# Kernel tuning notes

Measured on AMD Instinct MI355X. Metric: run time of the kernel, lower is better.

The kernel has to match this reference:

```python
import jax, jax.numpy as jnp
import numpy as np

HIDDEN = 1024
RANK = 4
N_TASKS = 5
LORA_SCALING = 1.0 / RANK  # lora_alpha / lora_rank = 1/4
LN_EPS = 1e-5


def setup_inputs() -> dict:
    key = jax.random.key(0)
    ks = jax.random.split(key, 9)
    B, S, D = 16, 2048, HIDDEN
    hidden_states = jax.random.normal(ks[0], (B, S, D), dtype=jnp.float32)
    input_tensor = jax.random.normal(ks[1], (B, S, D), dtype=jnp.float32)
    adapter_mask = jax.random.randint(ks[2], (B,), 0, N_TASKS, dtype=jnp.int32)
    W = jax.random.normal(ks[3], (D, D), dtype=jnp.float32) * 0.02
    b = jax.random.normal(ks[4], (D,), dtype=jnp.float32) * 0.02
    lora_A = jax.random.normal(ks[5], (N_TASKS, RANK, D), dtype=jnp.float32) * 0.02
    lora_B = jax.random.normal(ks[6], (N_TASKS, D, RANK), dtype=jnp.float32) * 0.02
    gamma = jnp.ones((D,), dtype=jnp.float32)
    beta = jnp.zeros((D,), dtype=jnp.float32)
    return {
        "hidden_states": hidden_states,
        "input_tensor": input_tensor,
        "W": W,
        "b": b,
        "lora_A": lora_A,
        "lora_B": lora_B,
        "gamma": gamma,
        "beta": beta,
        "adapter_mask": adapter_mask,
    }


def _layernorm(x, gamma, beta):
    mu = jnp.mean(x, axis=-1, keepdims=True)
    xc = x - mu
    var = jnp.mean(xc * xc, axis=-1, keepdims=True)
    return xc * jax.lax.rsqrt(var + LN_EPS) * gamma + beta


def reference(hidden_states, input_tensor, W, b, lora_A, lora_B, gamma, beta, adapter_mask):
    # Base dense projection (first self.dense call)
    h1 = jnp.einsum("bsd,ed->bse", hidden_states, W) + b  # [B,S,D]
    # Per-task LoRA-parametrized dense applied to the projected states
    # (the source loops over unique tasks with gather/scatter; vectorized here
    #  by gathering each batch row's adapter).
    base2 = jnp.einsum("bsd,ed->bse", h1, W) + b  # [B,S,D]
    A_b = lora_A[adapter_mask]  # [B, r, D]
    B_b = lora_B[adapter_mask]  # [B, D, r]
    low = jnp.einsum("bsd,brd->bsr", h1, A_b)  # [B,S,r]
    delta = jnp.einsum("bsr,bdr->bsd", low, B_b)  # [B,S,D]
    h2 = base2 + LORA_SCALING * delta
    # dropout is identity in eval / p=0; residual + LayerNorm
    return _layernorm(h2 + input_tensor, gamma, beta)
```

## Files before the change

kernel.cpp:

```cpp
#include <hip/hip_runtime.h>
#include <hip/hip_bf16.h>
#include <stdint.h>

#define D_HID 1024
#define M_TOT 32768
#define LN_EPS 1e-5f

typedef __bf16 bf16x8 __attribute__((ext_vector_type(8)));
typedef float f32x4 __attribute__((ext_vector_type(4)));
typedef unsigned short u16;
typedef u16 u16x8 __attribute__((ext_vector_type(8)));
typedef u16 u16x4v __attribute__((ext_vector_type(4)));

__device__ __forceinline__ float bf2f(u16 x) {
  union { unsigned int u; float f; } c; c.u = ((unsigned int)x) << 16; return c.f;
}
__device__ __forceinline__ u16 f2bf(float f) {
  union { __bf16 h; u16 u; } c; c.h = (__bf16)f; return c.u;
}
__device__ __forceinline__ u16x8 cvt8(const float* g) {
  float4 f0 = *(const float4*)g;
  float4 f1 = *(const float4*)(g + 4);
  u16x8 v;
  v[0] = f2bf(f0.x); v[1] = f2bf(f0.y); v[2] = f2bf(f0.z); v[3] = f2bf(f0.w);
  v[4] = f2bf(f1.x); v[5] = f2bf(f1.y); v[6] = f2bf(f1.z); v[7] = f2bf(f1.w);
  return v;
}
__device__ __forceinline__ void gld16(const u16* g, u16* lds_wave_base) {
  __builtin_amdgcn_global_load_lds(
      (__attribute__((address_space(1))) unsigned int*)g,
      (__attribute__((address_space(3))) unsigned int*)lds_wave_base, 16, 0, 0);
}

__global__ __launch_bounds__(256) void s1_prep(
    const float* __restrict__ hs, u16* __restrict__ hs_bf,
    const float* __restrict__ W, u16* __restrict__ hi, u16* __restrict__ lo,
    u16* __restrict__ hiT, u16* __restrict__ loT,
    const float* __restrict__ lA, u16* __restrict__ lAh, u16* __restrict__ lAl) {
  __shared__ float tile[32][33];
  const int bid = blockIdx.x, tid = threadIdx.x;
  if (bid < 2048) {
    int i = bid * 256 + tid;
#pragma unroll
    for (int it = 0; it < 8; ++it, i += 2048 * 256)
      *(u16x8*)(hs_bf + (size_t)i * 8) = cvt8(hs + (size_t)i * 8);
    return;
  }
  if (bid >= 3072) {
    const int b = bid - 3072;
    for (int i = tid; i < 16 * 1024; i += 256) {
      const int r = b * 16 + (i >> 10), c = i & 1023;
      const float v = (r < 20) ? lA[(size_t)r * 1024 + c] : 0.f;
      const u16 h = f2bf(v);
      lAh[(size_t)r * 1024 + c] = h;
      lAl[(size_t)r * 1024 + c] = f2bf(v - bf2f(h));
    }
    return;
  }
  const int rb = bid - 2048;
  const int bj = rb & 31, bi = rb >> 5;
  const int tx = tid & 31, ty = tid >> 5;
#pragma unroll
  for (int r0 = 0; r0 < 32; r0 += 8) {
    const int r = r0 + ty;
    const size_t o = (size_t)(bi * 32 + r) * D_HID + bj * 32 + tx;
    const float v = W[o];
    tile[r][tx] = v;
    const u16 h = f2bf(v);
    hi[o] = h; lo[o] = f2bf(v - bf2f(h));
  }
  __syncthreads();
#pragma unroll
  for (int r0 = 0; r0 < 32; r0 += 8) {
    const int r = r0 + ty;
    const float v = tile[tx][r];
    const size_t o = (size_t)(bj * 32 + r) * D_HID + bi * 32 + tx;
    const u16 h = f2bf(v);
    hiT[o] = h; loT[o] = f2bf(v - bf2f(h));
  }
}

__global__ __launch_bounds__(256) void s2_gemm(
    const u16* __restrict__ Ah, const u16* __restrict__ Al,
    const u16* __restrict__ Bh, const u16* __restrict__ Bl,
    const u16* __restrict__ lAh, const u16* __restrict__ lAl,
    float* __restrict__ C, float* __restrict__ A2) {
  __shared__ __align__(16) u16 smem[4][64 * 32];
  const int bid = blockIdx.x, tid = threadIdx.x;
  const int wave = tid >> 6, lane = tid & 63;
  const int by = bid >> 4, bx = bid & 15;
  const bool isA2 = (by == 16);
  const u16* Asel_h = isA2 ? lAh : Ah;
  const u16* Asel_l = isA2 ? lAl : Al;
  const int arow0 = isA2 ? 0 : by * 64;
  const u16* gsel = (wave == 0) ? Asel_h : (wave == 1) ? Asel_l
                  : (wave == 2) ? Bh : Bl;
  const int rb = (wave < 2) ? arow0 : bx * 64;
  const u16* gp = gsel + (size_t)(rb + (lane >> 2)) * D_HID + (lane & 3) * 8;
  u16* sb = &smem[wave][0];

  const int l15 = lane & 15, quad = lane >> 4;
  const int wm = wave >> 1, wn = wave & 1;
  const int fA = (wm * 32 + l15) * 32 + quad * 8;
  const int fB = (wn * 32 + l15) * 32 + quad * 8;
  f32x4 acc[2][2];
#pragma unroll
  for (int m = 0; m < 2; ++m)
#pragma unroll
    for (int n = 0; n < 2; ++n) acc[m][n] = (f32x4){0.f, 0.f, 0.f, 0.f};

  for (int k0 = 0; k0 < D_HID; k0 += 32) {
    __syncthreads();
#pragma unroll
    for (int q = 0; q < 4; ++q)
      gld16(gp + (size_t)q * 16 * D_HID, sb + q * 512);
    gp += 32;
    __syncthreads();
    bf16x8 ahf[2], alf[2], bhf[2], blf[2];
#pragma unroll
    for (int m = 0; m < 2; ++m) {
      ahf[m] = *(const bf16x8*)(&smem[0][fA + m * 512]);
      alf[m] = *(const bf16x8*)(&smem[1][fA + m * 512]);
    }
#pragma unroll
    for (int n = 0; n < 2; ++n) {
      bhf[n] = *(const bf16x8*)(&smem[2][fB + n * 512]);
      blf[n] = *(const bf16x8*)(&smem[3][fB + n * 512]);
    }
#pragma unroll
    for (int m = 0; m < 2; ++m)
#pragma unroll
      for (int n = 0; n < 2; ++n) {
        acc[m][n] = __builtin_amdgcn_mfma_f32_16x16x32_bf16(ahf[m], bhf[n], acc[m][n], 0, 0, 0);
        acc[m][n] = __builtin_amdgcn_mfma_f32_16x16x32_bf16(alf[m], bhf[n], acc[m][n], 0, 0, 0);
        acc[m][n] = __builtin_amdgcn_mfma_f32_16x16x32_bf16(ahf[m], blf[n], acc[m][n], 0, 0, 0);
      }
  }
  const int nn0 = bx * 64 + wn * 32;
#pragma unroll
  for (int m = 0; m < 2; ++m)
#pragma unroll
    for (int n = 0; n < 2; ++n) {
      const int nn = nn0 + n * 16 + l15;
#pragma unroll
      for (int r = 0; r < 4; ++r) {
        const int lr = wm * 32 + m * 16 + quad * 4 + r;
        if (!isA2) {
          C[(size_t)(by * 64 + lr) * D_HID + nn] = acc[m][n][r];
        } else if (lr < 20) {
          A2[(size_t)lr * D_HID + nn] = acc[m][n][r];
        }
      }
    }
}

__global__ __launch_bounds__(256) void weff_beff(
    const float* __restrict__ Wc, const float* __restrict__ A2,
    const float* __restrict__ lB, const float* __restrict__ lA,
    const float* __restrict__ W, const float* __restrict__ bvec,
    u16* __restrict__ Weff, float* __restrict__ beff) {
  const int n = blockIdx.x, t = blockIdx.y, tid = threadIdx.x;
  const int wave = tid >> 6, lane = tid & 63;
  float br[4];
#pragma unroll
  for (int r = 0; r < 4; ++r) br[r] = lB[(size_t)t * 4096 + n * 4 + r];
  float4 v = *(const float4*)(Wc + (size_t)n * D_HID + tid * 4);
#pragma unroll
  for (int r = 0; r < 4; ++r) {
    const float4 a2 = *(const float4*)(A2 + (size_t)(t * 4 + r) * D_HID + tid * 4);
    const float s = 0.25f * br[r];
    v.x += s * a2.x; v.y += s * a2.y; v.z += s * a2.z; v.w += s * a2.w;
  }
  u16x4v o; o[0] = f2bf(v.x); o[1] = f2bf(v.y); o[2] = f2bf(v.z); o[3] = f2bf(v.w);
  *(u16x4v*)(Weff + (size_t)t * 1048576 + (size_t)n * D_HID + tid * 4) = o;
  const float4 bb = *(const float4*)(bvec + tid * 4);
  float p[5];
  {
    const float4 wr = *(const float4*)(W + (size_t)n * D_HID + tid * 4);
    p[0] = wr.x * bb.x + wr.y * bb.y + wr.z * bb.z + wr.w * bb.w;
  }
#pragma unroll
  for (int r = 0; r < 4; ++r) {
    const float4 ar = *(const float4*)(lA + (size_t)(t * 4 + r) * D_HID + tid * 4);
    p[1 + r] = ar.x * bb.x + ar.y * bb.y + ar.z * bb.z + ar.w * bb.w;
  }
#pragma unroll
  for (int m = 1; m < 64; m <<= 1)
#pragma unroll
    for (int jj = 0; jj < 5; ++jj) p[jj] += __shfl_xor(p[jj], m);
  __shared__ float red[4][5];
  if (lane == 0)
#pragma unroll
    for (int jj = 0; jj < 5; ++jj) red[wave][jj] = p[jj];
  __syncthreads();
  if (tid == 0) {
    float P = 0.f, Cr[4] = {0.f, 0.f, 0.f, 0.f};
#pragma unroll
    for (int w = 0; w < 4; ++w) {
      P += red[w][0];
#pragma unroll
      for (int r = 0; r < 4; ++r) Cr[r] += red[w][1 + r];
    }
    const float e = br[0]*Cr[0] + br[1]*Cr[1] + br[2]*Cr[2] + br[3]*Cr[3];
    beff[t * D_HID + n] = P + bvec[n] + 0.25f * e;
  }
}

__global__ __launch_bounds__(512, 1) void gemm_main(
    const u16* __restrict__ Ag, const u16* __restrict__ Wf,
    const float* __restrict__ beff, const int* __restrict__ mask,
    float* __restrict__ out) {
  __shared__ __align__(16) u16 sAf[2 * 16384];
  __shared__ __align__(16) u16 sBf[2 * 16384];
  const int tid = threadIdx.x, wave = tid >> 6, lane = tid & 63;
  const int L = blockIdx.x;
  const int xcd = L & 7, j = L >> 3;
  const int bx = j & 3;
  const int by = xcd * 16 + (j >> 2);
  const int task = mask[by >> 3];
  const u16* Bg = Wf + (size_t)task * (D_HID * D_HID);

  const int acol = ((lane & 7) ^ (lane >> 3)) * 8;
  const int aBase = (by * 256 + wave * 8 + (lane >> 3)) * D_HID + acol;
  const int bBase = (bx * 256 + wave * 8 + (lane >> 3)) * D_HID + acol;

  auto stageA = [&](int ktar, int half) {
#pragma unroll
    for (int q = 0; q < 2; ++q)
      gld16(Ag + (aBase + ktar * 64 + half * 131072 + q * 65536),
            sAf + ((ktar & 1) * 16384 + half * 8192 + q * 4096 + wave * 512));
  };
  auto stageB = [&](int ktar, int half) {
#pragma unroll
    for (int q = 0; q < 2; ++q)
      gld16(Bg + (bBase + ktar * 64 + half * 131072 + q * 65536),
            sBf + ((ktar & 1) * 16384 + half * 8192 + q * 4096 + wave * 512));
  };

  const int wm = wave >> 2, wn = wave & 3;
  const int l15 = lane & 15, quad = lane >> 4, l7 = lane & 7;
  const int vA0 = (wm * 128 + l15) * 64 + ((quad ^ l7) * 8);
  const int vB0 = (wn * 64 + l15) * 64 + ((quad ^ l7) * 8);

  f32x4 acc[8][4];
#pragma unroll
  for (int i = 0; i < 8; ++i)
#pragma unroll
    for (int jn = 0; jn < 4; ++jn) acc[i][jn] = (f32x4){0.f, 0.f, 0.f, 0.f};

  stageB(0, 0); stageB(0, 1); stageA(0, 0); stageA(0, 1);
  stageB(1, 0); stageA(1, 0);
  asm volatile("s_waitcnt vmcnt(4)" ::: "memory");
  __builtin_amdgcn_s_barrier();
  __builtin_amdgcn_sched_barrier(0);

  bf16x8 a[4][2], b[4][2];
#pragma unroll 1
  for (int k2 = 0; k2 < 8; ++k2) {
#pragma unroll
    for (int par = 0; par < 2; ++par) {
      const int kt = k2 * 2 + par;
      const u16* pA = sAf + par * 16384;
      const u16* pB = sBf + par * 16384;
      const bool st01 = (par == 0) || (k2 < 7);
      const bool st23 = (k2 < 7);

#pragma unroll
      for (int m4 = 0; m4 < 4; ++m4) {
        a[m4][0] = *(const bf16x8*)(pA + (vA0 + m4 * 1024));
        a[m4][1] = *(const bf16x8*)(pA + ((vA0 ^ 32) + m4 * 1024));
      }
#pragma unroll
      for (int n2 = 0; n2 < 2; ++n2) {
        b[n2][0] = *(const bf16x8*)(pB + (vB0 + n2 * 1024));
        b[n2][1] = *(const bf16x8*)(pB + ((vB0 ^ 32) + n2 * 1024));
      }
      if (st01) stageB(kt + 1, 1);
      __builtin_amdgcn_s_barrier();
      asm volatile("s_waitcnt lgkmcnt(0)" ::: "memory");
      __builtin_amdgcn_sched_barrier(0);
      __builtin_amdgcn_s_setprio(1);
#pragma unroll
      for (int m4 = 0; m4 < 4; ++m4)
#pragma unroll
        for (int n2 = 0; n2 < 2; ++n2)
#pragma unroll
          for (int kk = 0; kk < 2; ++kk)
            acc[m4][n2] = __builtin_amdgcn_mfma_f32_16x16x32_bf16(
                a[m4][kk], b[n2][kk], acc[m4][n2], 0, 0, 0);
      __builtin_amdgcn_s_setprio(0);
      __builtin_amdgcn_s_barrier();
      __builtin_amdgcn_sched_barrier(0);

#pragma unroll
      for (int n2 = 0; n2 < 2; ++n2) {
        b[2 + n2][0] = *(const bf16x8*)(pB + (vB0 + (2 + n2) * 1024));
        b[2 + n2][1] = *(const bf16x8*)(pB + ((vB0 ^ 32) + (2 + n2) * 1024));
      }
      if (st01) stageA(kt + 1, 1);
      __builtin_amdgcn_s_barrier();
      asm volatile("s_waitcnt lgkmcnt(0)" ::: "memory");
      __builtin_amdgcn_sched_barrier(0);
      __builtin_amdgcn_s_setprio(1);
#pragma unroll
      for (int m4 = 0; m4 < 4; ++m4)
#pragma unroll
        for (int n2 = 0; n2 < 2; ++n2)
#pragma unroll
          for (int kk = 0; kk < 2; ++kk)
            acc[m4][2 + n2] = __builtin_amdgcn_mfma_f32_16x16x32_bf16(
                a[m4][kk], b[2 + n2][kk], acc[m4][2 + n2], 0, 0, 0);
      __builtin_amdgcn_s_setprio(0);
      __builtin_amdgcn_s_barrier();
      __builtin_amdgcn_sched_barrier(0);

#pragma unroll
      for (int m4 = 0; m4 < 4; ++m4) {
        a[m4][0] = *(const bf16x8*)(pA + (vA0 + (4 + m4) * 1024));
        a[m4][1] = *(const bf16x8*)(pA + ((vA0 ^ 32) + (4 + m4) * 1024));
      }
      if (st23) stageB(kt + 2, 0);
      __builtin_amdgcn_s_barrier();
      asm volatile("s_waitcnt lgkmcnt(0)" ::: "memory");
      __builtin_amdgcn_sched_barrier(0);
      __builtin_amdgcn_s_setprio(1);
#pragma unroll
      for (int m4 = 0; m4 < 4; ++m4)
#pragma unroll
        for (int n2 = 0; n2 < 2; ++n2)
#pragma unroll
          for (int kk = 0; kk < 2; ++kk)
            acc[4 + m4][n2] = __builtin_amdgcn_mfma_f32_16x16x32_bf16(
                a[m4][kk], b[n2][kk], acc[4 + m4][n2], 0, 0, 0);
      __builtin_amdgcn_s_setprio(0);
      __builtin_amdgcn_s_barrier();
      __builtin_amdgcn_sched_barrier(0);

      if (st23) stageA(kt + 2, 0);
      if (par == 0) {
        if (k2 < 7) { asm volatile("s_waitcnt vmcnt(4)" ::: "memory"); }
        else        { asm volatile("s_waitcnt vmcnt(0)" ::: "memory"); }
      } else {
        if (k2 < 7) { asm volatile("s_waitcnt vmcnt(4)" ::: "memory"); }
      }
      __builtin_amdgcn_s_barrier();
      asm volatile("s_waitcnt lgkmcnt(0)" ::: "memory");
      __builtin_amdgcn_sched_barrier(0);
      __builtin_amdgcn_s_setprio(1);
#pragma unroll
      for (int m4 = 0; m4 < 4; ++m4)
#pragma unroll
        for (int n2 = 0; n2 < 2; ++n2)
#pragma unroll
          for (int kk = 0; kk < 2; ++kk)
            acc[4 + m4][2 + n2] = __builtin_amdgcn_mfma_f32_16x16x32_bf16(
                a[m4][kk], b[2 + n2][kk], acc[4 + m4][2 + n2], 0, 0, 0);
      __builtin_amdgcn_s_setprio(0);
      __builtin_amdgcn_s_barrier();
      __builtin_amdgcn_sched_barrier(0);
    }
  }

  const float* bb = beff + task * D_HID;
  const size_t mBase = (size_t)by * 256 + wm * 128;
  const int nb0 = bx * 256 + wn * 64;
#pragma unroll
  for (int mf = 0; mf < 8; ++mf)
#pragma unroll
    for (int nf = 0; nf < 4; ++nf) {
      const int n = nb0 + nf * 16 + l15;
      const float bval = bb[n];
#pragma unroll
      for (int r = 0; r < 4; ++r) {
        const size_t m = mBase + mf * 16 + quad * 4 + r;
        out[m * D_HID + n] = acc[mf][nf][r] + bval;
      }
    }
}

__global__ __launch_bounds__(256) void ln4(float* __restrict__ io,
                                           const float* __restrict__ resid,
                                           const float* __restrict__ gamma,
                                           const float* __restrict__ beta) {
  const int row = blockIdx.x * 4 + (threadIdx.x >> 6);
  const int lane = threadIdx.x & 63;
  float* p = io + (size_t)row * D_HID + lane * 16;
  const float* rp = resid + (size_t)row * D_HID + lane * 16;
  float4 v0 = ((const float4*)p)[0], v1 = ((const float4*)p)[1];
  float4 v2 = ((const float4*)p)[2], v3 = ((const float4*)p)[3];
  float4 r0 = ((const float4*)rp)[0], r1 = ((const float4*)rp)[1];
  float4 r2 = ((const float4*)rp)[2], r3 = ((const float4*)rp)[3];
  v0.x += r0.x; v0.y += r0.y; v0.z += r0.z; v0.w += r0.w;
  v1.x += r1.x; v1.y += r1.y; v1.z += r1.z; v1.w += r1.w;
  v2.x += r2.x; v2.y += r2.y; v2.z += r2.z; v2.w += r2.w;
  v3.x += r3.x; v3.y += r3.y; v3.z += r3.z; v3.w += r3.w;
  float s = v0.x + v0.y + v0.z + v0.w + v1.x + v1.y + v1.z + v1.w
          + v2.x + v2.y + v2.z + v2.w + v3.x + v3.y + v3.z + v3.w;
  float q = v0.x*v0.x + v0.y*v0.y + v0.z*v0.z + v0.w*v0.w
          + v1.x*v1.x + v1.y*v1.y + v1.z*v1.z + v1.w*v1.w
          + v2.x*v2.x + v2.y*v2.y + v2.z*v2.z + v2.w*v2.w
          + v3.x*v3.x + v3.y*v3.y + v3.z*v3.z + v3.w*v3.w;
#pragma unroll
  for (int m = 1; m < 64; m <<= 1) { s += __shfl_xor(s, m); q += __shfl_xor(q, m); }
  const float mu  = s * (1.f / (float)D_HID);
  const float var = q * (1.f / (float)D_HID) - mu * mu;
  const float inv = rsqrtf(var + LN_EPS);
  const float4* gp = (const float4*)(gamma + lane * 16);
  const float4* bp = (const float4*)(beta + lane * 16);
  float4 g, bbv, o;
#define LNW(k, vk) \
  g = gp[k]; bbv = bp[k]; \
  o.x = (vk.x - mu) * inv * g.x + bbv.x; o.y = (vk.y - mu) * inv * g.y + bbv.y; \
  o.z = (vk.z - mu) * inv * g.z + bbv.z; o.w = (vk.w - mu) * inv * g.w + bbv.w; \
  ((float4*)p)[k] = o;
  LNW(0, v0) LNW(1, v1) LNW(2, v2) LNW(3, v3)
#undef LNW
}

extern "C" void kernel_launch(void* const* d_in, const int* in_sizes, int n_in,
                              void* d_out, int out_size, void* d_ws, size_t ws_size,
                              hipStream_t stream) {
  const float* hs    = (const float*)d_in[0];
  const float* inp   = (const float*)d_in[1];
  const float* W     = (const float*)d_in[2];
  const float* b     = (const float*)d_in[3];
  const float* lA    = (const float*)d_in[4];
  const float* lB    = (const float*)d_in[5];
  const float* gamma = (const float*)d_in[6];
  const float* beta  = (const float*)d_in[7];
  const int*   mask  = (const int*)d_in[8];
  float* out = (float*)d_out;

  char* wsb = (char*)d_ws;
  u16*   hs_bf = (u16*)wsb;
  float* Wc    = (float*)(wsb + 67108864);
  u16*   weff  = (u16*)(wsb + 71303168);
  u16*   Whi   = weff;
  u16*   Wlo   = weff + 1048576;
  u16*   WhiT  = weff + 2097152;
  u16*   WloT  = weff + 3145728;
  u16*   lAh   = weff + 4194304;
  u16*   lAl   = weff + 4325376;
  float* A2    = (float*)(wsb + 81788928);
  float* beff  = (float*)(wsb + 81871360);

  s1_prep<<<3080, 256, 0, stream>>>(hs, hs_bf, W, Whi, Wlo, WhiT, WloT, lA, lAh, lAl);
  s2_gemm<<<272, 256, 0, stream>>>(Whi, Wlo, WhiT, WloT, lAh, lAl, Wc, A2);
  weff_beff<<<dim3(1024, 5), 256, 0, stream>>>(Wc, A2, lB, lA, W, b, weff, beff);
  gemm_main<<<512, 512, 0, stream>>>(hs_bf, weff, beff, mask, out);
  ln4<<<M_TOT / 4, 256, 0, stream>>>(out, inp, gamma, beta);
}
```

Measured before the change: 504.7 us.

## Fuse fp32-to-bf16 conversion, main GEMM, residual and LayerNorm into one kernel

```diff
diff --git a/kernel.cpp b/kernel.cpp
--- a/kernel.cpp
+++ b/kernel.cpp
@@ -18,36 +18,20 @@
 __device__ __forceinline__ u16 f2bf(float f) {
   union { __bf16 h; u16 u; } c; c.h = (__bf16)f; return c.u;
 }
-__device__ __forceinline__ u16x8 cvt8(const float* g) {
-  float4 f0 = *(const float4*)g;
-  float4 f1 = *(const float4*)(g + 4);
-  u16x8 v;
-  v[0] = f2bf(f0.x); v[1] = f2bf(f0.y); v[2] = f2bf(f0.z); v[3] = f2bf(f0.w);
-  v[4] = f2bf(f1.x); v[5] = f2bf(f1.y); v[6] = f2bf(f1.z); v[7] = f2bf(f1.w);
-  return v;
-}
 __device__ __forceinline__ void gld16(const u16* g, u16* lds_wave_base) {
   __builtin_amdgcn_global_load_lds(
       (__attribute__((address_space(1))) unsigned int*)g,
       (__attribute__((address_space(3))) unsigned int*)lds_wave_base, 16, 0, 0);
 }
 
-__global__ __launch_bounds__(256) void s1_prep(
-    const float* __restrict__ hs, u16* __restrict__ hs_bf,
+__global__ __launch_bounds__(256) void prep_w(
     const float* __restrict__ W, u16* __restrict__ hi, u16* __restrict__ lo,
     u16* __restrict__ hiT, u16* __restrict__ loT,
     const float* __restrict__ lA, u16* __restrict__ lAh, u16* __restrict__ lAl) {
   __shared__ float tile[32][33];
   const int bid = blockIdx.x, tid = threadIdx.x;
-  if (bid < 2048) {
-    int i = bid * 256 + tid;
-#pragma unroll
-    for (int it = 0; it < 8; ++it, i += 2048 * 256)
-      *(u16x8*)(hs_bf + (size_t)i * 8) = cvt8(hs + (size_t)i * 8);
-    return;
-  }
-  if (bid >= 3072) {
-    const int b = bid - 3072;
+  if (bid >= 1024) {
+    const int b = bid - 1024;
     for (int i = tid; i < 16 * 1024; i += 256) {
       const int r = b * 16 + (i >> 10), c = i & 1023;
       const float v = (r < 20) ? lA[(size_t)r * 1024 + c] : 0.f;
@@ -57,8 +41,7 @@
     }
     return;
   }
-  const int rb = bid - 2048;
-  const int bj = rb & 31, bi = rb >> 5;
+  const int bj = bid & 31, bi = bid >> 5;
   const int tx = tid & 31, ty = tid >> 5;
 #pragma unroll
   for (int r0 = 0; r0 < 32; r0 += 8) {
@@ -206,215 +189,158 @@
   }
 }
 
-__global__ __launch_bounds__(512, 1) void gemm_main(
-    const u16* __restrict__ Ag, const u16* __restrict__ Wf,
-    const float* __restrict__ beff, const int* __restrict__ mask,
-    float* __restrict__ out) {
-  __shared__ __align__(16) u16 sAf[2 * 16384];
-  __shared__ __align__(16) u16 sBf[2 * 16384];
+__global__ __launch_bounds__(512, 1) void fused_main(
+    const float* __restrict__ hs, const u16* __restrict__ Wf,
+    const float* __restrict__ beff, const float* __restrict__ resid,
+    const int* __restrict__ mask, const float* __restrict__ gamma,
+    const float* __restrict__ beta, float* __restrict__ out) {
+  __shared__ __align__(16) u16 sB[2][32768];
+  __shared__ __align__(16) u16 sA[2][2048];
+  __shared__ float lnS[64][8], lnQ[64][8], lnMu[64], lnInv[64];
+
   const int tid = threadIdx.x, wave = tid >> 6, lane = tid & 63;
   const int L = blockIdx.x;
-  const int xcd = L & 7, j = L >> 3;
-  const int bx = j & 3;
-  const int by = xcd * 16 + (j >> 2);
-  const int task = mask[by >> 3];
-  const u16* Bg = Wf + (size_t)task * (D_HID * D_HID);
-
-  const int acol = ((lane & 7) ^ (lane >> 3)) * 8;
-  const int aBase = (by * 256 + wave * 8 + (lane >> 3)) * D_HID + acol;
-  const int bBase = (bx * 256 + wave * 8 + (lane >> 3)) * D_HID + acol;
-
-  auto stageA = [&](int ktar, int half) {
-#pragma unroll
-    for (int q = 0; q < 2; ++q)
-      gld16(Ag + (aBase + ktar * 64 + half * 131072 + q * 65536),
-            sAf + ((ktar & 1) * 16384 + half * 8192 + q * 4096 + wave * 512));
+  const int by = (L & 7) * 64 + (L >> 3);
+  const int m0 = by * 64;
+  const int task = mask[by >> 5];
+  const u16* Wt = Wf + (size_t)task * 1048576;
+
+  const int l8 = lane >> 3, s7 = lane & 7;
+  const int ob = s7 ^ l8;
+  const u16* gB = Wt + (size_t)(wave * 128 + 2 * l8 + (ob >> 2)) * D_HID
+                  + (ob & 3) * 8;
+  const float* gA = hs + (size_t)(m0 + wave * 8 + l8) * D_HID + s7 * 4;
+  const int aline = wave * 4 + (l8 >> 1);
+  const int aslot = ((l8 & 1) * 4 + (s7 >> 1)) ^ (aline & 7);
+  const int awAddr = aline * 64 + aslot * 8 + (s7 & 1) * 4;
+
+  const int l15 = lane & 15, quad = lane >> 4;
+  const int lh = l15 >> 1;
+  const int slotoff = ((((l15 & 1) * 4) + quad) ^ lh) * 8;
+  int vA[4], vB[8];
+#pragma unroll
+  for (int mf = 0; mf < 4; ++mf) vA[mf] = (mf * 8 + lh) * 64 + slotoff;
+#pragma unroll
+  for (int nf = 0; nf < 8; ++nf) vB[nf] = (wave * 64 + nf * 8 + lh) * 64 + slotoff;
+
+  f32x4 acc[4][8];
+#pragma unroll
+  for (int i = 0; i < 4; ++i)
+#pragma unroll
+    for (int j = 0; j < 8; ++j) acc[i][j] = (f32x4){0.f, 0.f, 0.f, 0.f};
+
+  auto stageB = [&](int kt) {
+    u16* dst = &sB[kt & 1][wave * 4096];
+    const u16* src = gB + kt * 32;
+#pragma unroll
+    for (int c = 0; c < 8; ++c)
+      gld16(src + c * 16 * D_HID, dst + c * 512);
   };
-  auto stageB = [&](int ktar, int half) {
-#pragma unroll
-    for (int q = 0; q < 2; ++q)
-      gld16(Bg + (bBase + ktar * 64 + half * 131072 + q * 65536),
-            sBf + ((ktar & 1) * 16384 + half * 8192 + q * 4096 + wave * 512));
-  };
-
-  const int wm = wave >> 2, wn = wave & 3;
-  const int l15 = lane & 15, quad = lane >> 4, l7 = lane & 7;
-  const int vA0 = (wm * 128 + l15) * 64 + ((quad ^ l7) * 8);
-  const int vB0 = (wn * 64 + l15) * 64 + ((quad ^ l7) * 8);
-
-  f32x4 acc[8][4];
-#pragma unroll
-  for (int i = 0; i < 8; ++i)
-#pragma unroll
-    for (int jn = 0; jn < 4; ++jn) acc[i][jn] = (f32x4){0.f, 0.f, 0.f, 0.f};
-
-  stageB(0, 0); stageB(0, 1); stageA(0, 0); stageA(0, 1);
-  stageB(1, 0); stageA(1, 0);
-  asm volatile("s_waitcnt vmcnt(4)" ::: "memory");
-  __builtin_amdgcn_s_barrier();
-  __builtin_amdgcn_sched_barrier(0);
-
-  bf16x8 a[4][2], b[4][2];
-#pragma unroll 1
-  for (int k2 = 0; k2 < 8; ++k2) {
-#pragma unroll
-    for (int par = 0; par < 2; ++par) {
-      const int kt = k2 * 2 + par;
-      const u16* pA = sAf + par * 16384;
-      const u16* pB = sBf + par * 16384;
-      const bool st01 = (par == 0) || (k2 < 7);
-      const bool st23 = (k2 < 7);
-
-#pragma unroll
-      for (int m4 = 0; m4 < 4; ++m4) {
-        a[m4][0] = *(const bf16x8*)(pA + (vA0 + m4 * 1024));
-        a[m4][1] = *(const bf16x8*)(pA + ((vA0 ^ 32) + m4 * 1024));
-      }
-#pragma unroll
-      for (int n2 = 0; n2 < 2; ++n2) {
-        b[n2][0] = *(const bf16x8*)(pB + (vB0 + n2 * 1024));
-        b[n2][1] = *(const bf16x8*)(pB + ((vB0 ^ 32) + n2 * 1024));
-      }
-      if (st01) stageB(kt + 1, 1);
-      __builtin_amdgcn_s_barrier();
-      asm volatile("s_waitcnt lgkmcnt(0)" ::: "memory");
-      __builtin_amdgcn_sched_barrier(0);
-      __builtin_amdgcn_s_setprio(1);
-#pragma unroll
-      for (int m4 = 0; m4 < 4; ++m4)
-#pragma unroll
-        for (int n2 = 0; n2 < 2; ++n2)
-#pragma unroll
-          for (int kk = 0; kk < 2; ++kk)
-            acc[m4][n2] = __builtin_amdgcn_mfma_f32_16x16x32_bf16(
-                a[m4][kk], b[n2][kk], acc[m4][n2], 0, 0, 0);
-      __builtin_amdgcn_s_setprio(0);
-      __builtin_amdgcn_s_barrier();
-      __builtin_amdgcn_sched_barrier(0);
-
-#pragma unroll
-      for (int n2 = 0; n2 < 2; ++n2) {
-        b[2 + n2][0] = *(const bf16x8*)(pB + (vB0 + (2 + n2) * 1024));
-        b[2 + n2][1] = *(const bf16x8*)(pB + ((vB0 ^ 32) + (2 + n2) * 1024));
-      }
-      if (st01) stageA(kt + 1, 1);
-      __builtin_amdgcn_s_barrier();
-      asm volatile("s_waitcnt lgkmcnt(0)" ::: "memory");
-      __builtin_amdgcn_sched_barrier(0);
-      __builtin_amdgcn_s_setprio(1);
-#pragma unroll
-      for (int m4 = 0; m4 < 4; ++m4)
-#pragma unroll
-        for (int n2 = 0; n2 < 2; ++n2)
-#pragma unroll
-          for (int kk = 0; kk < 2; ++kk)
-            acc[m4][2 + n2] = __builtin_amdgcn_mfma_f32_16x16x32_bf16(
-                a[m4][kk], b[2 + n2][kk], acc[m4][2 + n2], 0, 0, 0);
-      __builtin_amdgcn_s_setprio(0);
-      __builtin_amdgcn_s_barrier();
-      __builtin_amdgcn_sched_barrier(0);
-
-#pragma unroll
-      for (int m4 = 0; m4 < 4; ++m4) {
-        a[m4][0] = *(const bf16x8*)(pA + (vA0 + (4 + m4) * 1024));
-        a[m4][1] = *(const bf16x8*)(pA + ((vA0 ^ 32) + (4 + m4) * 1024));
-      }
-      if (st23) stageB(kt + 2, 0);
-      __builtin_amdgcn_s_barrier();
-      asm volatile("s_waitcnt lgkmcnt(0)" ::: "memory");
-      __builtin_amdgcn_sched_barrier(0);
-      __builtin_amdgcn_s_setprio(1);
-#pragma unroll
-      for (int m4 = 0; m4 < 4; ++m4)
-#pragma unroll
-        for (int n2 = 0; n2 < 2; ++n2)
-#pragma unroll
-          for (int kk = 0; kk < 2; ++kk)
-            acc[4 + m4][n2] = __builtin_amdgcn_mfma_f32_16x16x32_bf16(
-                a[m4][kk], b[n2][kk], acc[4 + m4][n2], 0, 0, 0);
-      __builtin_amdgcn_s_setprio(0);
-      __builtin_amdgcn_s_barrier();
-      __builtin_amdgcn_sched_barrier(0);
-
-      if (st23) stageA(kt + 2, 0);
-      if (par == 0) {
-        if (k2 < 7) { asm volatile("s_waitcnt vmcnt(4)" ::: "memory"); }
-        else        { asm volatile("s_waitcnt vmcnt(0)" ::: "memory"); }
-      } else {
-        if (k2 < 7) { asm volatile("s_waitcnt vmcnt(4)" ::: "memory"); }
-      }
-      __builtin_amdgcn_s_barrier();
-      asm volatile("s_waitcnt lgkmcnt(0)" ::: "memory");
-      __builtin_amdgcn_sched_barrier(0);
-      __builtin_amdgcn_s_setprio(1);
-#pragma unroll
-      for (int m4 = 0; m4 < 4; ++m4)
-#pragma unroll
-        for (int n2 = 0; n2 < 2; ++n2)
-#pragma unroll
-          for (int kk = 0; kk < 2; ++kk)
-            acc[4 + m4][2 + n2] = __builtin_amdgcn_mfma_f32_16x16x32_bf16(
-                a[m4][kk], b[2 + n2][kk], acc[4 + m4][2 + n2], 0, 0, 0);
-      __builtin_amdgcn_s_setprio(0);
-      __builtin_amdgcn_s_barrier();
-      __builtin_amdgcn_sched_barrier(0);
-    }
-  }
-
-  const float* bb = beff + task * D_HID;
-  const size_t mBase = (size_t)by * 256 + wm * 128;
-  const int nb0 = bx * 256 + wn * 64;
-#pragma unroll
-  for (int mf = 0; mf < 8; ++mf)
-#pragma unroll
-    for (int nf = 0; nf < 4; ++nf) {
-      const int n = nb0 + nf * 16 + l15;
-      const float bval = bb[n];
-#pragma unroll
-      for (int r = 0; r < 4; ++r) {
-        const size_t m = mBase + mf * 16 + quad * 4 + r;
-        out[m * D_HID + n] = acc[mf][nf][r] + bval;
-      }
-    }
-}
-
-__global__ __launch_bounds__(256) void ln4(float* __restrict__ io,
-                                           const float* __restrict__ resid,
-                                           const float* __restrict__ gamma,
-                                           const float* __restrict__ beta) {
-  const int row = blockIdx.x * 4 + (threadIdx.x >> 6);
-  const int lane = threadIdx.x & 63;
-  float* p = io + (size_t)row * D_HID + lane * 16;
-  const float* rp = resid + (size_t)row * D_HID + lane * 16;
-  float4 v0 = ((const float4*)p)[0], v1 = ((const float4*)p)[1];
-  float4 v2 = ((const float4*)p)[2], v3 = ((const float4*)p)[3];
-  float4 r0 = ((const float4*)rp)[0], r1 = ((const float4*)rp)[1];
-  float4 r2 = ((const float4*)rp)[2], r3 = ((const float4*)rp)[3];
-  v0.x += r0.x; v0.y += r0.y; v0.z += r0.z; v0.w += r0.w;
-  v1.x += r1.x; v1.y += r1.y; v1.z += r1.z; v1.w += r1.w;
-  v2.x += r2.x; v2.y += r2.y; v2.z += r2.z; v2.w += r2.w;
-  v3.x += r3.x; v3.y += r3.y; v3.z += r3.z; v3.w += r3.w;
-  float s = v0.x + v0.y + v0.z + v0.w + v1.x + v1.y + v1.z + v1.w
-          + v2.x + v2.y + v2.z + v2.w + v3.x + v3.y + v3.z + v3.w;
-  float q = v0.x*v0.x + v0.y*v0.y + v0.z*v0.z + v0.w*v0.w
-          + v1.x*v1.x + v1.y*v1.y + v1.z*v1.z + v1.w*v1.w
-          + v2.x*v2.x + v2.y*v2.y + v2.z*v2.z + v2.w*v2.w
-          + v3.x*v3.x + v3.y*v3.y + v3.z*v3.z + v3.w*v3.w;
-#pragma unroll
-  for (int m = 1; m < 64; m <<= 1) { s += __shfl_xor(s, m); q += __shfl_xor(q, m); }
-  const float mu  = s * (1.f / (float)D_HID);
-  const float var = q * (1.f / (float)D_HID) - mu * mu;
-  const float inv = rsqrtf(var + LN_EPS);
-  const float4* gp = (const float4*)(gamma + lane * 16);
-  const float4* bp = (const float4*)(beta + lane * 16);
-  float4 g, bbv, o;
-#define LNW(k, vk) \
-  g = gp[k]; bbv = bp[k]; \
-  o.x = (vk.x - mu) * inv * g.x + bbv.x; o.y = (vk.y - mu) * inv * g.y + bbv.y; \
-  o.z = (vk.z - mu) * inv * g.z + bbv.z; o.w = (vk.w - mu) * inv * g.w + bbv.w; \
-  ((float4*)p)[k] = o;
-  LNW(0, v0) LNW(1, v1) LNW(2, v2) LNW(3, v3)
-#undef LNW
+
+  {
+    float4 a4 = *(const float4*)gA;
+    stageB(0);
+    u16x4v aw;
+    aw[0] = f2bf(a4.x); aw[1] = f2bf(a4.y); aw[2] = f2bf(a4.z); aw[3] = f2bf(a4.w);
+    *(u16x4v*)&sA[0][awAddr] = aw;
+  }
+  __syncthreads();
+
+#pragma unroll 2
+  for (int t = 0; t < 32; ++t) {
+    const int cur = t & 1;
+    const bool st = (t < 31);
+    float4 a4n;
+    if (st) {
+      a4n = *(const float4*)(gA + (t + 1) * 32);
+      stageB(t + 1);
+    }
+    bf16x8 af[4], bfr[8];
+#pragma unroll
+    for (int mf = 0; mf < 4; ++mf) af[mf] = *(const bf16x8*)&sA[cur][vA[mf]];
+#pragma unroll
+    for (int nf = 0; nf < 8; ++nf) bfr[nf] = *(const bf16x8*)&sB[cur][vB[nf]];
+    __builtin_amdgcn_s_setprio(1);
+#pragma unroll
+    for (int mf = 0; mf < 4; ++mf)
+#pragma unroll
+      for (int nf = 0; nf < 8; ++nf)
+        acc[mf][nf] = __builtin_amdgcn_mfma_f32_16x16x32_bf16(
+            af[mf], bfr[nf], acc[mf][nf], 0, 0, 0);
+    __builtin_amdgcn_s_setprio(0);
+    if (st) {
+      u16x4v aw;
+      aw[0] = f2bf(a4n.x); aw[1] = f2bf(a4n.y);
+      aw[2] = f2bf(a4n.z); aw[3] = f2bf(a4n.w);
+      *(u16x4v*)&sA[cur ^ 1][awAddr] = aw;
+      __syncthreads();
+    }
+  }
+
+  const float* bb = beff + (size_t)task * D_HID;
+  const int colb = wave * 128 + l15;
+  float bval[8];
+#pragma unroll
+  for (int nf = 0; nf < 8; ++nf) bval[nf] = bb[colb + nf * 16];
+#pragma unroll
+  for (int mf = 0; mf < 4; ++mf) {
+#pragma unroll
+    for (int r = 0; r < 4; ++r) {
+      const size_t rowg = (size_t)(m0 + mf * 16 + quad * 4 + r) * D_HID + colb;
+      float rs[8];
+#pragma unroll
+      for (int nf = 0; nf < 8; ++nf) rs[nf] = resid[rowg + nf * 16];
+#pragma unroll
+      for (int nf = 0; nf < 8; ++nf)
+        acc[mf][nf][r] += bval[nf] + rs[nf];
+    }
+  }
+#pragma unroll
+  for (int mf = 0; mf < 4; ++mf)
+#pragma unroll
+    for (int r = 0; r < 4; ++r) {
+      float s = 0.f, q = 0.f;
+#pragma unroll
+      for (int nf = 0; nf < 8; ++nf) {
+        const float v = acc[mf][nf][r];
+        s += v; q = fmaf(v, v, q);
+      }
+#pragma unroll
+      for (int msk = 1; msk < 16; msk <<= 1) {
+        s += __shfl_xor(s, msk); q += __shfl_xor(q, msk);
+      }
+      if (l15 == 0) {
+        const int row = mf * 16 + quad * 4 + r;
+        lnS[row][wave] = s; lnQ[row][wave] = q;
+      }
+    }
+  __syncthreads();
+  if (tid < 64) {
+    float ts = 0.f, tq = 0.f;
+#pragma unroll
+    for (int w = 0; w < 8; ++w) { ts += lnS[tid][w]; tq += lnQ[tid][w]; }
+    const float mu = ts * (1.f / (float)D_HID);
+    const float var = tq * (1.f / (float)D_HID) - mu * mu;
+    lnMu[tid] = mu; lnInv[tid] = rsqrtf(var + LN_EPS);
+  }
+  __syncthreads();
+  float gv[8], bv[8];
+#pragma unroll
+  for (int nf = 0; nf < 8; ++nf) {
+    gv[nf] = gamma[colb + nf * 16];
+    bv[nf] = beta[colb + nf * 16];
+  }
+#pragma unroll
+  for (int mf = 0; mf < 4; ++mf)
+#pragma unroll
+    for (int r = 0; r < 4; ++r) {
+      const int row = mf * 16 + quad * 4 + r;
+      const float mu = lnMu[row], inv = lnInv[row];
+      const size_t rowg = (size_t)(m0 + row) * D_HID + colb;
+#pragma unroll
+      for (int nf = 0; nf < 8; ++nf)
+        out[rowg + nf * 16] = (acc[mf][nf][r] - mu) * inv * gv[nf] + bv[nf];
+    }
 }
 
 extern "C" void kernel_launch(void* const* d_in, const int* in_sizes, int n_in,
@@ -432,21 +358,19 @@
   float* out = (float*)d_out;
 
   char* wsb = (char*)d_ws;
-  u16*   hs_bf = (u16*)wsb;
-  float* Wc    = (float*)(wsb + 67108864);
-  u16*   weff  = (u16*)(wsb + 71303168);
+  float* Wc    = (float*)wsb;
+  u16*   weff  = (u16*)(wsb + 4194304);
   u16*   Whi   = weff;
   u16*   Wlo   = weff + 1048576;
   u16*   WhiT  = weff + 2097152;
   u16*   WloT  = weff + 3145728;
   u16*   lAh   = weff + 4194304;
   u16*   lAl   = weff + 4325376;
-  float* A2    = (float*)(wsb + 81788928);
-  float* beff  = (float*)(wsb + 81871360);
-
-  s1_prep<<<3080, 256, 0, stream>>>(hs, hs_bf, W, Whi, Wlo, WhiT, WloT, lA, lAh, lAl);
+  float* A2    = (float*)(wsb + 14680064);
+  float* beff  = (float*)(wsb + 14811136);
+
+  prep_w<<<1032, 256, 0, stream>>>(W, Whi, Wlo, WhiT, WloT, lA, lAh, lAl);
   s2_gemm<<<272, 256, 0, stream>>>(Whi, Wlo, WhiT, WloT, lAh, lAl, Wc, A2);
   weff_beff<<<dim3(1024, 5), 256, 0, stream>>>(Wc, A2, lB, lA, W, b, weff, beff);
-  gemm_main<<<512, 512, 0, stream>>>(hs_bf, weff, beff, mask, out);
-  ln4<<<M_TOT / 4, 256, 0, stream>>>(out, inp, gamma, beta);
-}
+  fused_main<<<512, 512, 0, stream>>>(hs, weff, beff, inp, mask, gamma, beta, out);
+}
```

Result: slower. 524.8 us (+4.0%).

## Fuse fp32-to-bf16 conversion of hidden states into main GEMM A-tile loading

Applied to the files above, without the earlier changes.

```diff
diff --git a/kernel.cpp b/kernel.cpp
--- a/kernel.cpp
+++ b/kernel.cpp
@@ -18,36 +18,20 @@
 __device__ __forceinline__ u16 f2bf(float f) {
   union { __bf16 h; u16 u; } c; c.h = (__bf16)f; return c.u;
 }
-__device__ __forceinline__ u16x8 cvt8(const float* g) {
-  float4 f0 = *(const float4*)g;
-  float4 f1 = *(const float4*)(g + 4);
-  u16x8 v;
-  v[0] = f2bf(f0.x); v[1] = f2bf(f0.y); v[2] = f2bf(f0.z); v[3] = f2bf(f0.w);
-  v[4] = f2bf(f1.x); v[5] = f2bf(f1.y); v[6] = f2bf(f1.z); v[7] = f2bf(f1.w);
-  return v;
-}
 __device__ __forceinline__ void gld16(const u16* g, u16* lds_wave_base) {
   __builtin_amdgcn_global_load_lds(
       (__attribute__((address_space(1))) unsigned int*)g,
       (__attribute__((address_space(3))) unsigned int*)lds_wave_base, 16, 0, 0);
 }
 
-__global__ __launch_bounds__(256) void s1_prep(
-    const float* __restrict__ hs, u16* __restrict__ hs_bf,
+__global__ __launch_bounds__(256) void prep_w(
     const float* __restrict__ W, u16* __restrict__ hi, u16* __restrict__ lo,
     u16* __restrict__ hiT, u16* __restrict__ loT,
     const float* __restrict__ lA, u16* __restrict__ lAh, u16* __restrict__ lAl) {
   __shared__ float tile[32][33];
   const int bid = blockIdx.x, tid = threadIdx.x;
-  if (bid < 2048) {
-    int i = bid * 256 + tid;
-#pragma unroll
-    for (int it = 0; it < 8; ++it, i += 2048 * 256)
-      *(u16x8*)(hs_bf + (size_t)i * 8) = cvt8(hs + (size_t)i * 8);
-    return;
-  }
-  if (bid >= 3072) {
-    const int b = bid - 3072;
+  if (bid >= 1024) {
+    const int b = bid - 1024;
     for (int i = tid; i < 16 * 1024; i += 256) {
       const int r = b * 16 + (i >> 10), c = i & 1023;
       const float v = (r < 20) ? lA[(size_t)r * 1024 + c] : 0.f;
@@ -57,8 +41,7 @@
     }
     return;
   }
-  const int rb = bid - 2048;
-  const int bj = rb & 31, bi = rb >> 5;
+  const int bj = bid & 31, bi = bid >> 5;
   const int tx = tid & 31, ty = tid >> 5;
 #pragma unroll
   for (int r0 = 0; r0 < 32; r0 += 8) {
@@ -207,7 +190,7 @@
 }
 
 __global__ __launch_bounds__(512, 1) void gemm_main(
-    const u16* __restrict__ Ag, const u16* __restrict__ Wf,
+    const float* __restrict__ hs, const u16* __restrict__ Wf,
     const float* __restrict__ beff, const int* __restrict__ mask,
     float* __restrict__ out) {
   __shared__ __align__(16) u16 sAf[2 * 16384];
@@ -220,16 +203,8 @@
   const int task = mask[by >> 3];
   const u16* Bg = Wf + (size_t)task * (D_HID * D_HID);
 
-  const int acol = ((lane & 7) ^ (lane >> 3)) * 8;
-  const int aBase = (by * 256 + wave * 8 + (lane >> 3)) * D_HID + acol;
-  const int bBase = (bx * 256 + wave * 8 + (lane >> 3)) * D_HID + acol;
-
-  auto stageA = [&](int ktar, int half) {
-#pragma unroll
-    for (int q = 0; q < 2; ++q)
-      gld16(Ag + (aBase + ktar * 64 + half * 131072 + q * 65536),
-            sAf + ((ktar & 1) * 16384 + half * 8192 + q * 4096 + wave * 512));
-  };
+  const int l8 = lane >> 3, s7 = lane & 7;
+  const int bBase = (bx * 256 + wave * 8 + l8) * D_HID + (s7 ^ l8) * 8;
   auto stageB = [&](int ktar, int half) {
 #pragma unroll
     for (int q = 0; q < 2; ++q)
@@ -237,6 +212,29 @@
             sBf + ((ktar & 1) * 16384 + half * 8192 + q * 4096 + wave * 512));
   };
 
+  const float* gA = hs + (size_t)(by * 256 + wave * 8 + l8) * D_HID + (s7 ^ l8) * 8;
+  const int awBase = wave * 512 + l8 * 64 + s7 * 8;
+  f32x4 av[8];
+  auto ALOAD = [&](int kt) {
+#pragma unroll
+    for (int i = 0; i < 4; ++i) {
+      const float* p = gA + (size_t)i * 64 * D_HID + kt * 64;
+      av[2 * i]     = *(const f32x4*)p;
+      av[2 * i + 1] = *(const f32x4*)(p + 4);
+    }
+  };
+  auto AWRITE = [&](int kt) {
+#pragma unroll
+    for (int i = 0; i < 4; ++i) {
+      u16x8 o;
+      o[0] = f2bf(av[2 * i][0]);     o[1] = f2bf(av[2 * i][1]);
+      o[2] = f2bf(av[2 * i][2]);     o[3] = f2bf(av[2 * i][3]);
+      o[4] = f2bf(av[2 * i + 1][0]); o[5] = f2bf(av[2 * i + 1][1]);
+      o[6] = f2bf(av[2 * i + 1][2]); o[7] = f2bf(av[2 * i + 1][3]);
+      *(u16x8*)&sAf[(kt & 1) * 16384 + i * 4096 + awBase] = o;
+    }
+  };
+
   const int wm = wave >> 2, wn = wave & 3;
   const int l15 = lane & 15, quad = lane >> 4, l7 = lane & 7;
   const int vA0 = (wm * 128 + l15) * 64 + ((quad ^ l7) * 8);
@@ -248,9 +246,10 @@
 #pragma unroll
     for (int jn = 0; jn < 4; ++jn) acc[i][jn] = (f32x4){0.f, 0.f, 0.f, 0.f};
 
-  stageB(0, 0); stageB(0, 1); stageA(0, 0); stageA(0, 1);
-  stageB(1, 0); stageA(1, 0);
-  asm volatile("s_waitcnt vmcnt(4)" ::: "memory");
+  ALOAD(0);
+  stageB(0, 0); stageB(0, 1); stageB(1, 0);
+  AWRITE(0);
+  asm volatile("s_waitcnt vmcnt(2) lgkmcnt(0)" ::: "memory");
   __builtin_amdgcn_s_barrier();
   __builtin_amdgcn_sched_barrier(0);
 
@@ -275,7 +274,7 @@
         b[n2][0] = *(const bf16x8*)(pB + (vB0 + n2 * 1024));
         b[n2][1] = *(const bf16x8*)(pB + ((vB0 ^ 32) + n2 * 1024));
       }
-      if (st01) stageB(kt + 1, 1);
+      if (st01) { stageB(kt + 1, 1); ALOAD(kt + 1); }
       __builtin_amdgcn_s_barrier();
       asm volatile("s_waitcnt lgkmcnt(0)" ::: "memory");
       __builtin_amdgcn_sched_barrier(0);
@@ -297,7 +296,6 @@
         b[2 + n2][0] = *(const bf16x8*)(pB + (vB0 + (2 + n2) * 1024));
         b[2 + n2][1] = *(const bf16x8*)(pB + ((vB0 ^ 32) + (2 + n2) * 1024));
       }
-      if (st01) stageA(kt + 1, 1);
       __builtin_amdgcn_s_barrier();
       asm volatile("s_waitcnt lgkmcnt(0)" ::: "memory");
       __builtin_amdgcn_sched_barrier(0);
@@ -336,13 +334,9 @@
       __builtin_amdgcn_s_barrier();
       __builtin_amdgcn_sched_barrier(0);
 
-      if (st23) stageA(kt + 2, 0);
-      if (par == 0) {
-        if (k2 < 7) { asm volatile("s_waitcnt vmcnt(4)" ::: "memory"); }
-        else        { asm volatile("s_waitcnt vmcnt(0)" ::: "memory"); }
-      } else {
-        if (k2 < 7) { asm volatile("s_waitcnt vmcnt(4)" ::: "memory"); }
-      }
+      if (kt < 14)       { asm volatile("s_waitcnt vmcnt(2)" ::: "memory"); }
+      else if (kt == 14) { asm volatile("s_waitcnt vmcnt(0)" ::: "memory"); }
+      if (st01) AWRITE(kt + 1);
       __builtin_amdgcn_s_barrier();
       asm volatile("s_waitcnt lgkmcnt(0)" ::: "memory");
       __builtin_amdgcn_sched_barrier(0);
@@ -432,21 +426,20 @@
   float* out = (float*)d_out;
 
   char* wsb = (char*)d_ws;
-  u16*   hs_bf = (u16*)wsb;
-  float* Wc    = (float*)(wsb + 67108864);
-  u16*   weff  = (u16*)(wsb + 71303168);
+  float* Wc    = (float*)wsb;
+  u16*   weff  = (u16*)(wsb + 4194304);
   u16*   Whi   = weff;
   u16*   Wlo   = weff + 1048576;
   u16*   WhiT  = weff + 2097152;
   u16*   WloT  = weff + 3145728;
   u16*   lAh   = weff + 4194304;
   u16*   lAl   = weff + 4325376;
-  float* A2    = (float*)(wsb + 81788928);
-  float* beff  = (float*)(wsb + 81871360);
-
-  s1_prep<<<3080, 256, 0, stream>>>(hs, hs_bf, W, Whi, Wlo, WhiT, WloT, lA, lAh, lAl);
+  float* A2    = (float*)(wsb + 14680064);
+  float* beff  = (float*)(wsb + 14811136);
+
+  prep_w<<<1032, 256, 0, stream>>>(W, Whi, Wlo, WhiT, WloT, lA, lAh, lAl);
   s2_gemm<<<272, 256, 0, stream>>>(Whi, Wlo, WhiT, WloT, lAh, lAl, Wc, A2);
   weff_beff<<<dim3(1024, 5), 256, 0, stream>>>(Wc, A2, lB, lA, W, b, weff, beff);
-  gemm_main<<<512, 512, 0, stream>>>(hs_bf, weff, beff, mask, out);
+  gemm_main<<<512, 512, 0, stream>>>(hs, weff, beff, mask, out);
   ln4<<<M_TOT / 4, 256, 0, stream>>>(out, inp, gamma, beta);
 }
```

New measurement: 500.2 us. Within noise of the previous version (-0.9%).
